# Optimization experiments

Hardware: AMD Instinct MI355X
Metric: run time of the kernel (lower is better)

The kernel has to match this reference:

```python
import jax, jax.numpy as jnp
import numpy as np

N, E = 50000, 800000
C_IN, C_OUT, DIM, K = 64, 64, 3, 2
EPS = 1e-5


def setup_inputs() -> dict:
    key = jax.random.key(0)
    k1, k2, k3, k4, k5 = jax.random.split(key, 5)
    x = jax.random.normal(k1, (N, C_IN), dtype=jnp.float32)
    edge_index = jax.random.randint(k2, (2, E), 0, N, dtype=jnp.int32)
    edge_attr = jax.random.uniform(k3, (E, DIM), dtype=jnp.float32)  # pseudo coords in [0,1]
    W = jax.random.normal(k4, (K ** DIM, C_IN, C_OUT), dtype=jnp.float32) * 0.05
    root = jax.random.normal(k5, (C_IN, C_OUT), dtype=jnp.float32) * 0.05
    gamma = jnp.ones((C_OUT,), dtype=jnp.float32)
    beta = jnp.zeros((C_OUT,), dtype=jnp.float32)
    return {"x": x, "edge_attr": edge_attr, "W": W, "root": root,
            "gamma": gamma, "beta": beta, "edge_index": edge_index}


def _spline_basis(edge_attr):
    """Degree-1 open B-spline basis. Returns (weights [E,2^D], kernel idx [E,2^D])."""
    D = edge_attr.shape[1]
    v = edge_attr * (K - 1)                      # [E, D]
    k0 = jnp.floor(v)
    frac = v - k0                                # in [0,1)
    k0 = k0.astype(jnp.int32)
    bits = np.stack(np.unravel_index(np.arange(2 ** D), (2,) * D), axis=-1).astype(np.int32)  # [2^D, D]
    bits_f = jnp.asarray(bits, dtype=edge_attr.dtype)
    # per-dim weight: frac if bit else (1 - frac); product over dims
    w = jnp.where(bits_f[None] > 0, frac[:, None, :], 1.0 - frac[:, None, :])  # [E, 2^D, D]
    weights = jnp.prod(w, axis=-1)               # [E, 2^D]
    idx_d = jnp.clip(k0[:, None, :] + bits[None], 0, K - 1)  # [E, 2^D, D]
    radix = jnp.asarray(K ** np.arange(D), dtype=jnp.int32)
    idx = jnp.sum(idx_d * radix, axis=-1)        # [E, 2^D] in [0, K^D)
    return weights, idx


def reference(x, edge_attr, W, root, gamma, beta, edge_index):
    src, dst = edge_index[0], edge_index[1]
    Etot = edge_attr.shape[0]
    S = W.shape[0]  # K^D

    weights, idx = _spline_basis(edge_attr)      # [E, 2^D] each
    # dense per-edge basis over all K^D kernel slots
    B = jnp.zeros((Etot, S), dtype=x.dtype).at[jnp.arange(Etot)[:, None], idx].add(weights)

    xj = x[src]                                  # [E, C_in] gather
    z = (B[:, :, None] * xj[:, None, :]).reshape(Etot, S * x.shape[1])  # [E, S*C_in]
    msg = z @ W.reshape(S * x.shape[1], W.shape[2])                     # [E, C_out]

    agg = jax.ops.segment_sum(msg, dst, num_segments=x.shape[0])        # scatter-add
    cnt = jax.ops.segment_sum(jnp.ones((Etot,), dtype=x.dtype), dst, num_segments=x.shape[0])
    out = agg / jnp.maximum(cnt, 1.0)[:, None] + x @ root               # mean aggr + root weight

    # BatchNorm over nodes (training-mode batch stats)
    mean = jnp.mean(out, axis=0)
    var = jnp.var(out, axis=0)
    y = (out - mean) * jax.lax.rsqrt(var + EPS) * gamma + beta
    return jax.nn.elu(y)
```

## Files before the change

kernel.cpp:

```cpp
#include <hip/hip_runtime.h>
#include <hip/hip_bf16.h>
#include <cstdint>
#include <cstddef>

#define NN 50000
#define NE 800000
#define EPS 1e-5f

typedef short bf16x8 __attribute__((ext_vector_type(8)));
typedef float f32x4  __attribute__((ext_vector_type(4)));
typedef float f32x2  __attribute__((ext_vector_type(2)));


#define NB_WT   144
#define NB_CNT  3125
#define NB_MFMA 1564
#define NB_SCAN 25

static __device__ __forceinline__ ushort f2bf(float f) {
    __hip_bfloat16 h = __float2bfloat16(f);
    return *reinterpret_cast<ushort*>(&h);
}
static __device__ __forceinline__ uint32_t pack2(float a, float b) {
    return (uint32_t)f2bf(a) | ((uint32_t)f2bf(b) << 16);
}

__global__ __launch_bounds__(256) void prep_count_k(const float* __restrict__ W,
                                                    const float* __restrict__ root,
                                                    ushort* __restrict__ WTg,
                                                    const int* __restrict__ ei,
                                                    int* __restrict__ deg,
                                                    int* __restrict__ rank) {
    const int b = blockIdx.x;
    if (b < NB_WT) {
        const int idx = b * 256 + threadIdx.x;
        const int s  = idx >> 12;
        const int co = (idx >> 6) & 63;
        const int ci = idx & 63;
        const float v = (s < 8) ? W[s * 4096 + ci * 64 + co] : root[ci * 64 + co];
        WTg[idx] = f2bf(v);
    } else {
        const int e = (b - NB_WT) * 256 + threadIdx.x;
        if (e < NE) rank[e] = atomicAdd(&deg[ei[NE + e]], 1);
    }
}

__global__ __launch_bounds__(256) void mfma_scan_k(
        const float* __restrict__ x, const ushort* __restrict__ WTg,
        uint8_t* __restrict__ H8, float* __restrict__ Hroot,
        const int* __restrict__ deg, int* __restrict__ offs,
        int* __restrict__ part) {
    __shared__ __align__(16) ushort XA[64 * 64];
    __shared__ __align__(16) ushort WT[5 * 64 * 64];
    __shared__ int sh[256];
    const int t = threadIdx.x;
    const int b = blockIdx.x;

    if (b >= NB_MFMA) {
        const int sb = b - NB_MFMA;
        const int base = sb * 2048 + t * 8;
        int v[8]; int sum = 0;
        #pragma unroll
        for (int k = 0; k < 8; ++k) {
            int i = base + k;
            int d = (i < NN) ? deg[i] : 0;
            v[k] = sum; sum += d;
        }
        sh[t] = sum; __syncthreads();
        for (int off = 1; off < 256; off <<= 1) {
            int val = sh[t];
            int add = (t >= off) ? sh[t - off] : 0;
            __syncthreads();
            sh[t] = val + add;
            __syncthreads();
        }
        int excl = (t > 0) ? sh[t - 1] : 0;
        #pragma unroll
        for (int k = 0; k < 8; ++k) {
            int i = base + k;
            if (i < NN) offs[i] = excl + v[k];
        }
        if (t == 255) part[sb] = sh[255];
        return;
    }

    const int bx   = (b < 782) ? b : b - 782;
    const int half = (b < 782) ? 0 : 1;
    const int n0 = bx * 64;
    const int sbeg   = half ? 5 : 0;
    const int scount = half ? 4 : 5;

    #pragma unroll
    for (int rep = 0; rep < 2; ++rep) {
        const int vt   = rep * 256 + t;
        const int row  = vt >> 3;
        const int col8 = vt & 7;
        const int n = n0 + row;
        uint4 u;
        if (n < NN) {
            const float4 v0 = *(const float4*)&x[(size_t)n * 64 + col8 * 8];
            const float4 v1 = *(const float4*)&x[(size_t)n * 64 + col8 * 8 + 4];
            u.x = pack2(v0.x, v0.y); u.y = pack2(v0.z, v0.w);
            u.z = pack2(v1.x, v1.y); u.w = pack2(v1.z, v1.w);
        } else {
            u = make_uint4(0, 0, 0, 0);
        }
        const int idx = (row * 64 + col8 * 8) ^ ((row & 7) << 3);
        *(uint4*)&XA[idx] = u;
    }
    const int nchunk = scount * 512;
    for (int c = t; c < nchunk; c += 256) {
        const int row  = c >> 3;
        const int col8 = c & 7;
        const uint4 u = *(const uint4*)&WTg[(size_t)(sbeg * 64 + row) * 64 + col8 * 8];
        const int idx = (row * 64 + col8 * 8) ^ ((row & 7) << 3);
        *(uint4*)&WT[idx] = u;
    }
    __syncthreads();

    const int w    = t >> 6;
    const int lane = t & 63;
    const int mrow = lane & 15;
    const int kgrp = lane >> 4;
    const int swz  = (mrow & 7) << 3;
    const int arow = w * 16 + mrow;
    const int n    = n0 + arow;

    const bf16x8 a0 = *(const bf16x8*)&XA[((arow * 64) + 0 * 32 + kgrp * 8) ^ swz];
    const bf16x8 a1 = *(const bf16x8*)&XA[((arow * 64) + 1 * 32 + kgrp * 8) ^ swz];

    for (int sl = 0; sl < scount; ++sl) {
        const int s = sbeg + sl;
        const ushort* wt = &WT[sl * 4096];
        f32x4 acc[4];
        #pragma unroll
        for (int ct = 0; ct < 4; ++ct) {
            acc[ct] = (f32x4){0.f, 0.f, 0.f, 0.f};
            const int brow = ct * 16 + mrow;
            const bf16x8 b0 = *(const bf16x8*)&wt[((brow * 64) + 0 * 32 + kgrp * 8) ^ swz];
            const bf16x8 b1 = *(const bf16x8*)&wt[((brow * 64) + 1 * 32 + kgrp * 8) ^ swz];
            acc[ct] = __builtin_amdgcn_mfma_f32_16x16x32_bf16(b0, a0, acc[ct], 0, 0, 0);
            acc[ct] = __builtin_amdgcn_mfma_f32_16x16x32_bf16(b1, a1, acc[ct], 0, 0, 0);
        }
        if (n < NN) {
            if (s < 8) {
                #pragma unroll
                for (int ct = 0; ct < 4; ++ct) {
                    int p = __builtin_amdgcn_cvt_pk_fp8_f32(acc[ct][0], acc[ct][1], 0, false);
                    p     = __builtin_amdgcn_cvt_pk_fp8_f32(acc[ct][2], acc[ct][3], p, true);
                    *(uint32_t*)&H8[(size_t)n * 512 + s * 64 + ct * 16 + kgrp * 4] = (uint32_t)p;
                }
            } else {
                #pragma unroll
                for (int ct = 0; ct < 4; ++ct) {
                    *(float4*)&Hroot[(size_t)n * 64 + ct * 16 + kgrp * 4] =
                        make_float4(acc[ct][0], acc[ct][1], acc[ct][2], acc[ct][3]);
                }
            }
        }
    }
}

__global__ __launch_bounds__(256) void scatter_k(const int* __restrict__ ei,
                                                 const float* __restrict__ attr,
                                                 const int* __restrict__ offs,
                                                 const int* __restrict__ part,
                                                 const int* __restrict__ rank,
                                                 int2* __restrict__ recs) {
    __shared__ int pp[25];
    const int t = threadIdx.x;
    if (t < 25) pp[t] = part[t];
    __syncthreads();
    if (t == 0) {
        int s = 0;
        #pragma unroll
        for (int i = 0; i < 25; ++i) { int v = pp[i]; pp[i] = s; s += v; }
    }
    __syncthreads();
    int e = blockIdx.x * 256 + t;
    if (e >= NE) return;
    const int src = ei[e];
    const int dst = ei[NE + e];
    const float f0 = attr[(size_t)e * 3 + 0];
    const float f1 = attr[(size_t)e * 3 + 1];
    const float f2 = attr[(size_t)e * 3 + 2];
    const uint32_t q = (uint32_t)rintf(f0 * 1023.f)
                     | ((uint32_t)rintf(f1 * 1023.f) << 10)
                     | ((uint32_t)rintf(f2 * 1023.f) << 20);
    const int p = offs[dst] + pp[dst >> 11] + rank[e];
    recs[p] = make_int2(src, (int)q);
}

__global__ __launch_bounds__(256) void aggregate_k(const int* __restrict__ offs,
                                                   const int* __restrict__ part,
                                                   const int* __restrict__ deg,
                                                   const int2* __restrict__ recs,
                                                   const uint8_t* __restrict__ H8,
                                                   const float* __restrict__ Hroot,
                                                   float* __restrict__ outb,
                                                   float* __restrict__ bnps,
                                                   float* __restrict__ bnpq) {
    __shared__ int pp[25];
    __shared__ float red_s[4][64], red_q[4][64];
    const int t = threadIdx.x, lane = t & 63, w = t >> 6;
    if (t < 25) pp[t] = part[t];
    __syncthreads();
    if (t == 0) {
        int s = 0;
        #pragma unroll
        for (int i = 0; i < 25; ++i) { int v = pp[i]; pp[i] = s; s += v; }
    }
    __syncthreads();

    const int n = blockIdx.x * 4 + w;
    const int sidx = lane >> 3;
    const int cog  = lane & 7;
    const float sg0 = (sidx & 1) ? 1.f : -1.f, cc0 = (sidx & 1) ? 0.f : 1.f;
    const float sg1 = (sidx & 2) ? 1.f : -1.f, cc1 = (sidx & 2) ? 0.f : 1.f;
    const float sg2 = (sidx & 4) ? 1.f : -1.f, cc2 = (sidx & 4) ? 0.f : 1.f;
    const int cnt = deg[n];
    const int beg = offs[n] + pp[n >> 11];
    const int2* rp = recs + beg;
    const size_t loff = (size_t)(lane << 3);

    f32x2 acc2[4] = {(f32x2){0.f, 0.f}, (f32x2){0.f, 0.f},
                     (f32x2){0.f, 0.f}, (f32x2){0.f, 0.f}};

#define DECODE_W(qv, wv)                                                     \
    {                                                                        \
        const uint32_t q_ = (uint32_t)(qv);                                  \
        const float f0_ = (float)(q_ & 1023u) * (1.f / 1023.f);              \
        const float f1_ = (float)((q_ >> 10) & 1023u) * (1.f / 1023.f);      \
        const float f2_ = (float)((q_ >> 20) & 1023u) * (1.f / 1023.f);      \
        wv = (cc0 + sg0 * f0_) * ((cc1 + sg1 * f1_) * (cc2 + sg2 * f2_));    \
    }
#define ACCUM(wv, h)                                                         \
    {                                                                        \
        const f32x2 w2_ = {wv, wv};                                          \
        acc2[0] += w2_ * (f32x2)__builtin_amdgcn_cvt_pk_f32_fp8((int)(h).x, false); \
        acc2[1] += w2_ * (f32x2)__builtin_amdgcn_cvt_pk_f32_fp8((int)(h).x, true);  \
        acc2[2] += w2_ * (f32x2)__builtin_amdgcn_cvt_pk_f32_fp8((int)(h).y, false); \
        acc2[3] += w2_ * (f32x2)__builtin_amdgcn_cvt_pk_f32_fp8((int)(h).y, true);  \
    }

    int j = 0;
    for (; j + 3 < cnt; j += 4) {
        const int2 r0 = rp[j];
        const int2 r1 = rp[j + 1];
        const int2 r2 = rp[j + 2];
        const int2 r3 = rp[j + 3];
        const uint2 h0 = *(const uint2*)(H8 + (size_t)r0.x * 512 + loff);
        const uint2 h1 = *(const uint2*)(H8 + (size_t)r1.x * 512 + loff);
        const uint2 h2 = *(const uint2*)(H8 + (size_t)r2.x * 512 + loff);
        const uint2 h3 = *(const uint2*)(H8 + (size_t)r3.x * 512 + loff);
        float w0, w1, w2, w3;
        DECODE_W(r0.y, w0); DECODE_W(r1.y, w1);
        DECODE_W(r2.y, w2); DECODE_W(r3.y, w3);
        ACCUM(w0, h0); ACCUM(w1, h1); ACCUM(w2, h2); ACCUM(w3, h3);
    }
    for (; j < cnt; ++j) {
        const int2 r0 = rp[j];
        const uint2 h0 = *(const uint2*)(H8 + (size_t)r0.x * 512 + loff);
        float w0;
        DECODE_W(r0.y, w0);
        ACCUM(w0, h0);
    }
#undef DECODE_W
#undef ACCUM

    float accf[8] = {acc2[0].x, acc2[0].y, acc2[1].x, acc2[1].y,
                     acc2[2].x, acc2[2].y, acc2[3].x, acc2[3].y};
    #pragma unroll
    for (int k = 0; k < 8; ++k) {
        float v = accf[k];
        v += __shfl_xor(v, 8, 64);
        v += __shfl_xor(v, 16, 64);
        v += __shfl_xor(v, 32, 64);
        accf[k] = v;
    }
    if (sidx == 0) {
        const float inv = 1.f / fmaxf((float)cnt, 1.f);
        const size_t base = (size_t)n * 64 + cog * 8;
        const float4 r0 = *(const float4*)&Hroot[base];
        const float4 r1 = *(const float4*)&Hroot[base + 4];
        float vv[8];
        vv[0] = accf[0] * inv + r0.x; vv[1] = accf[1] * inv + r0.y;
        vv[2] = accf[2] * inv + r0.z; vv[3] = accf[3] * inv + r0.w;
        vv[4] = accf[4] * inv + r1.x; vv[5] = accf[5] * inv + r1.y;
        vv[6] = accf[6] * inv + r1.z; vv[7] = accf[7] * inv + r1.w;
        *(float4*)&outb[base]     = make_float4(vv[0], vv[1], vv[2], vv[3]);
        *(float4*)&outb[base + 4] = make_float4(vv[4], vv[5], vv[6], vv[7]);
        #pragma unroll
        for (int k = 0; k < 8; ++k) {
            red_s[w][cog * 8 + k] = vv[k];
            red_q[w][cog * 8 + k] = vv[k] * vv[k];
        }
    }
    __syncthreads();
    if (t < 64) {
        const float s = red_s[0][t] + red_s[1][t] + red_s[2][t] + red_s[3][t];
        const float q = red_q[0][t] + red_q[1][t] + red_q[2][t] + red_q[3][t];
        const int slot = (blockIdx.x & 63) * 64 + t;
        atomicAdd(&bnps[slot], s);
        atomicAdd(&bnpq[slot], q);
    }
}

__global__ __launch_bounds__(256) void finalize_kernel(float* __restrict__ outb,
                                                       const float* __restrict__ bnps,
                                                       const float* __restrict__ bnpq,
                                                       const float* __restrict__ gamma,
                                                       const float* __restrict__ beta) {
    __shared__ float sc_sh[64], sh_sh[64];
    const int t = threadIdx.x;
    if (t < 64) {
        float s = 0.f, q = 0.f;
        for (int k = 0; k < 64; ++k) { s += bnps[k * 64 + t]; q += bnpq[k * 64 + t]; }
        const float mean = s * (1.f / NN);
        const float var  = q * (1.f / NN) - mean * mean;
        const float sc = rsqrtf(var + EPS) * gamma[t];
        sc_sh[t] = sc;
        sh_sh[t] = beta[t] - mean * sc;
    }
    __syncthreads();
    const int total4 = NN * 16;
    for (int idx = blockIdx.x * 256 + t; idx < total4; idx += gridDim.x * 256) {
        float4 v = ((const float4*)outb)[idx];
        const int co0 = (idx & 15) * 4;
        float o[4] = {v.x, v.y, v.z, v.w};
        #pragma unroll
        for (int j = 0; j < 4; ++j) {
            const float y = o[j] * sc_sh[co0 + j] + sh_sh[co0 + j];
            o[j] = (y > 0.f) ? y : expm1f(y);
        }
        ((float4*)outb)[idx] = make_float4(o[0], o[1], o[2], o[3]);
    }
}

extern "C" void kernel_launch(void* const* d_in, const int* in_sizes, int n_in,
                              void* d_out, int out_size, void* d_ws, size_t ws_size,
                              hipStream_t stream) {
    const float* x     = (const float*)d_in[0];
    const float* attr  = (const float*)d_in[1];
    const float* W     = (const float*)d_in[2];
    const float* root  = (const float*)d_in[3];
    const float* gamma = (const float*)d_in[4];
    const float* beta  = (const float*)d_in[5];
    const int*   ei    = (const int*)d_in[6];
    float* outb = (float*)d_out;

    char* ws = (char*)d_ws;
    uint8_t* H8    = (uint8_t*)(ws);
    float*   Hroot = (float*)(ws + 25600000);
    int2*    recs  = (int2*)(ws + 38400000);
    int*     rank  = (int*)(ws + 44800000);
    int*     offs  = (int*)(ws + 48000000);
    int*     deg   = (int*)(ws + 48200000);
    int*     part  = (int*)(ws + 48400000);
    float*   bnps  = (float*)(ws + 48400128);
    float*   bnpq  = (float*)(ws + 48416512);
    ushort*  WTg   = (ushort*)(ws + 48432896);

    hipMemsetAsync(ws + 48200000, 0, 232896, stream);

    prep_count_k<<<NB_WT + NB_CNT, 256, 0, stream>>>(W, root, WTg, ei, deg, rank);
    mfma_scan_k<<<NB_MFMA + NB_SCAN, 256, 0, stream>>>(x, WTg, H8, Hroot, deg, offs, part);
    scatter_k<<<NB_CNT, 256, 0, stream>>>(ei, attr, offs, part, rank, recs);
    aggregate_k<<<NN / 4, 256, 0, stream>>>(offs, part, deg, recs, H8, Hroot, outb, bnps, bnpq);
    finalize_kernel<<<256, 256, 0, stream>>>(outb, bnps, bnpq, gamma, beta);
}
```

Baseline: 175.3 us.

## Store root projection in bf16 and merge MFMA halves into one block

The x@root result is now stored as bf16 instead of fp32, which halves its write and read traffic between the MFMA and aggregate kernels. Each MFMA block now handles all 9 weight slices in two sequential passes that reload the shared weight tile, so x is loaded and converted only once per node tile, at the cost of half as many blocks. BatchNorm partial buffers are zeroed inside the prep kernel instead of by the memset, and the shared-memory reduction layout is transposed to reduce bank conflicts. Rounding the root term to bf16 adds a small amount of precision loss.

Measured after the change: 167.8 us. 4.3% less time.

```diff
diff --git a/kernel.cpp b/kernel.cpp
--- a/kernel.cpp
+++ b/kernel.cpp
@@ -14,12 +14,18 @@
 
 #define NB_WT   144
 #define NB_CNT  3125
-#define NB_MFMA 1564
+#define NB_MFMA 782
 #define NB_SCAN 25
 
 static __device__ __forceinline__ ushort f2bf(float f) {
     __hip_bfloat16 h = __float2bfloat16(f);
     return *reinterpret_cast<ushort*>(&h);
+}
+static __device__ __forceinline__ float bf_lo(uint32_t u) {
+    return __uint_as_float(u << 16);
+}
+static __device__ __forceinline__ float bf_hi(uint32_t u) {
+    return __uint_as_float(u & 0xffff0000u);
 }
 static __device__ __forceinline__ uint32_t pack2(float a, float b) {
     return (uint32_t)f2bf(a) | ((uint32_t)f2bf(b) << 16);
@@ -30,7 +36,9 @@
                                                     ushort* __restrict__ WTg,
                                                     const int* __restrict__ ei,
                                                     int* __restrict__ deg,
-                                                    int* __restrict__ rank) {
+                                                    int* __restrict__ rank,
+                                                    float* __restrict__ bnps,
+                                                    float* __restrict__ bnpq) {
     const int b = blockIdx.x;
     if (b < NB_WT) {
         const int idx = b * 256 + threadIdx.x;
@@ -39,6 +47,7 @@
         const int ci = idx & 63;
         const float v = (s < 8) ? W[s * 4096 + ci * 64 + co] : root[ci * 64 + co];
         WTg[idx] = f2bf(v);
+        if (idx < 4096) { bnps[idx] = 0.f; bnpq[idx] = 0.f; }
     } else {
         const int e = (b - NB_WT) * 256 + threadIdx.x;
         if (e < NE) rank[e] = atomicAdd(&deg[ei[NE + e]], 1);
@@ -47,7 +56,7 @@
 
 __global__ __launch_bounds__(256) void mfma_scan_k(
         const float* __restrict__ x, const ushort* __restrict__ WTg,
-        uint8_t* __restrict__ H8, float* __restrict__ Hroot,
+        uint8_t* __restrict__ H8, ushort* __restrict__ Hrootb,
         const int* __restrict__ deg, int* __restrict__ offs,
         int* __restrict__ part) {
     __shared__ __align__(16) ushort XA[64 * 64];
@@ -84,11 +93,7 @@
         return;
     }
 
-    const int bx   = (b < 782) ? b : b - 782;
-    const int half = (b < 782) ? 0 : 1;
-    const int n0 = bx * 64;
-    const int sbeg   = half ? 5 : 0;
-    const int scount = half ? 4 : 5;
+    const int n0 = b * 64;
 
     #pragma unroll
     for (int rep = 0; rep < 2; ++rep) {
@@ -108,15 +113,6 @@
         const int idx = (row * 64 + col8 * 8) ^ ((row & 7) << 3);
         *(uint4*)&XA[idx] = u;
     }
-    const int nchunk = scount * 512;
-    for (int c = t; c < nchunk; c += 256) {
-        const int row  = c >> 3;
-        const int col8 = c & 7;
-        const uint4 u = *(const uint4*)&WTg[(size_t)(sbeg * 64 + row) * 64 + col8 * 8];
-        const int idx = (row * 64 + col8 * 8) ^ ((row & 7) << 3);
-        *(uint4*)&WT[idx] = u;
-    }
-    __syncthreads();
 
     const int w    = t >> 6;
     const int lane = t & 63;
@@ -125,39 +121,57 @@
     const int swz  = (mrow & 7) << 3;
     const int arow = w * 16 + mrow;
     const int n    = n0 + arow;
-
-    const bf16x8 a0 = *(const bf16x8*)&XA[((arow * 64) + 0 * 32 + kgrp * 8) ^ swz];
-    const bf16x8 a1 = *(const bf16x8*)&XA[((arow * 64) + 1 * 32 + kgrp * 8) ^ swz];
-
-    for (int sl = 0; sl < scount; ++sl) {
-        const int s = sbeg + sl;
-        const ushort* wt = &WT[sl * 4096];
-        f32x4 acc[4];
-        #pragma unroll
-        for (int ct = 0; ct < 4; ++ct) {
-            acc[ct] = (f32x4){0.f, 0.f, 0.f, 0.f};
-            const int brow = ct * 16 + mrow;
-            const bf16x8 b0 = *(const bf16x8*)&wt[((brow * 64) + 0 * 32 + kgrp * 8) ^ swz];
-            const bf16x8 b1 = *(const bf16x8*)&wt[((brow * 64) + 1 * 32 + kgrp * 8) ^ swz];
-            acc[ct] = __builtin_amdgcn_mfma_f32_16x16x32_bf16(b0, a0, acc[ct], 0, 0, 0);
-            acc[ct] = __builtin_amdgcn_mfma_f32_16x16x32_bf16(b1, a1, acc[ct], 0, 0, 0);
-        }
-        if (n < NN) {
-            if (s < 8) {
-                #pragma unroll
-                for (int ct = 0; ct < 4; ++ct) {
-                    int p = __builtin_amdgcn_cvt_pk_fp8_f32(acc[ct][0], acc[ct][1], 0, false);
-                    p     = __builtin_amdgcn_cvt_pk_fp8_f32(acc[ct][2], acc[ct][3], p, true);
-                    *(uint32_t*)&H8[(size_t)n * 512 + s * 64 + ct * 16 + kgrp * 4] = (uint32_t)p;
-                }
-            } else {
-                #pragma unroll
-                for (int ct = 0; ct < 4; ++ct) {
-                    *(float4*)&Hroot[(size_t)n * 64 + ct * 16 + kgrp * 4] =
-                        make_float4(acc[ct][0], acc[ct][1], acc[ct][2], acc[ct][3]);
+    bf16x8 a0, a1;
+
+    for (int pass = 0; pass < 2; ++pass) {
+        const int sbeg   = pass ? 5 : 0;
+        const int scount = pass ? 4 : 5;
+        const int nchunk = scount * 512;
+        for (int c = t; c < nchunk; c += 256) {
+            const int row  = c >> 3;
+            const int col8 = c & 7;
+            const uint4 u = *(const uint4*)&WTg[(size_t)(sbeg * 64 + row) * 64 + col8 * 8];
+            const int idx = (row * 64 + col8 * 8) ^ ((row & 7) << 3);
+            *(uint4*)&WT[idx] = u;
+        }
+        __syncthreads();
+        if (pass == 0) {
+            a0 = *(const bf16x8*)&XA[((arow * 64) + 0 * 32 + kgrp * 8) ^ swz];
+            a1 = *(const bf16x8*)&XA[((arow * 64) + 1 * 32 + kgrp * 8) ^ swz];
+        }
+        for (int sl = 0; sl < scount; ++sl) {
+            const int s = sbeg + sl;
+            const ushort* wt = &WT[sl * 4096];
+            f32x4 acc[4];
+            #pragma unroll
+            for (int ct = 0; ct < 4; ++ct) {
+                acc[ct] = (f32x4){0.f, 0.f, 0.f, 0.f};
+                const int brow = ct * 16 + mrow;
+                const bf16x8 b0 = *(const bf16x8*)&wt[((brow * 64) + 0 * 32 + kgrp * 8) ^ swz];
+                const bf16x8 b1 = *(const bf16x8*)&wt[((brow * 64) + 1 * 32 + kgrp * 8) ^ swz];
+                acc[ct] = __builtin_amdgcn_mfma_f32_16x16x32_bf16(b0, a0, acc[ct], 0, 0, 0);
+                acc[ct] = __builtin_amdgcn_mfma_f32_16x16x32_bf16(b1, a1, acc[ct], 0, 0, 0);
+            }
+            if (n < NN) {
+                if (s < 8) {
+                    #pragma unroll
+                    for (int ct = 0; ct < 4; ++ct) {
+                        int p = __builtin_amdgcn_cvt_pk_fp8_f32(acc[ct][0], acc[ct][1], 0, false);
+                        p     = __builtin_amdgcn_cvt_pk_fp8_f32(acc[ct][2], acc[ct][3], p, true);
+                        *(uint32_t*)&H8[(size_t)n * 512 + s * 64 + ct * 16 + kgrp * 4] = (uint32_t)p;
+                    }
+                } else {
+                    #pragma unroll
+                    for (int ct = 0; ct < 4; ++ct) {
+                        ushort4 h4;
+                        h4.x = f2bf(acc[ct][0]); h4.y = f2bf(acc[ct][1]);
+                        h4.z = f2bf(acc[ct][2]); h4.w = f2bf(acc[ct][3]);
+                        *(ushort4*)&Hrootb[(size_t)n * 64 + ct * 16 + kgrp * 4] = h4;
+                    }
                 }
             }
         }
+        __syncthreads();
     }
 }
 
@@ -196,7 +210,7 @@
                                                    const int* __restrict__ deg,
                                                    const int2* __restrict__ recs,
                                                    const uint8_t* __restrict__ H8,
-                                                   const float* __restrict__ Hroot,
+                                                   const ushort* __restrict__ Hrootb,
                                                    float* __restrict__ outb,
                                                    float* __restrict__ bnps,
                                                    float* __restrict__ bnpq) {
@@ -281,26 +295,26 @@
     if (sidx == 0) {
         const float inv = 1.f / fmaxf((float)cnt, 1.f);
         const size_t base = (size_t)n * 64 + cog * 8;
-        const float4 r0 = *(const float4*)&Hroot[base];
-        const float4 r1 = *(const float4*)&Hroot[base + 4];
+        const uint4 hr = *(const uint4*)&Hrootb[base];
+        const float rr[8] = {bf_lo(hr.x), bf_hi(hr.x), bf_lo(hr.y), bf_hi(hr.y),
+                             bf_lo(hr.z), bf_hi(hr.z), bf_lo(hr.w), bf_hi(hr.w)};
         float vv[8];
-        vv[0] = accf[0] * inv + r0.x; vv[1] = accf[1] * inv + r0.y;
-        vv[2] = accf[2] * inv + r0.z; vv[3] = accf[3] * inv + r0.w;
-        vv[4] = accf[4] * inv + r1.x; vv[5] = accf[5] * inv + r1.y;
-        vv[6] = accf[6] * inv + r1.z; vv[7] = accf[7] * inv + r1.w;
+        #pragma unroll
+        for (int k = 0; k < 8; ++k) vv[k] = accf[k] * inv + rr[k];
         *(float4*)&outb[base]     = make_float4(vv[0], vv[1], vv[2], vv[3]);
         *(float4*)&outb[base + 4] = make_float4(vv[4], vv[5], vv[6], vv[7]);
         #pragma unroll
         for (int k = 0; k < 8; ++k) {
-            red_s[w][cog * 8 + k] = vv[k];
-            red_q[w][cog * 8 + k] = vv[k] * vv[k];
+            red_s[w][k * 8 + cog] = vv[k];
+            red_q[w][k * 8 + cog] = vv[k] * vv[k];
         }
     }
     __syncthreads();
     if (t < 64) {
         const float s = red_s[0][t] + red_s[1][t] + red_s[2][t] + red_s[3][t];
         const float q = red_q[0][t] + red_q[1][t] + red_q[2][t] + red_q[3][t];
-        const int slot = (blockIdx.x & 63) * 64 + t;
+        const int co = (t & 7) * 8 + (t >> 3);
+        const int slot = (blockIdx.x & 63) * 64 + co;
         atomicAdd(&bnps[slot], s);
         atomicAdd(&bnpq[slot], q);
     }
@@ -350,22 +364,22 @@
     float* outb = (float*)d_out;
 
     char* ws = (char*)d_ws;
-    uint8_t* H8    = (uint8_t*)(ws);
-    float*   Hroot = (float*)(ws + 25600000);
-    int2*    recs  = (int2*)(ws + 38400000);
-    int*     rank  = (int*)(ws + 44800000);
-    int*     offs  = (int*)(ws + 48000000);
-    int*     deg   = (int*)(ws + 48200000);
-    int*     part  = (int*)(ws + 48400000);
-    float*   bnps  = (float*)(ws + 48400128);
-    float*   bnpq  = (float*)(ws + 48416512);
-    ushort*  WTg   = (ushort*)(ws + 48432896);
-
-    hipMemsetAsync(ws + 48200000, 0, 232896, stream);
-
-    prep_count_k<<<NB_WT + NB_CNT, 256, 0, stream>>>(W, root, WTg, ei, deg, rank);
-    mfma_scan_k<<<NB_MFMA + NB_SCAN, 256, 0, stream>>>(x, WTg, H8, Hroot, deg, offs, part);
+    uint8_t* H8     = (uint8_t*)(ws);
+    ushort*  Hrootb = (ushort*)(ws + 25600000);
+    int2*    recs   = (int2*)(ws + 32000000);
+    int*     rank   = (int*)(ws + 38400000);
+    int*     offs   = (int*)(ws + 41600000);
+    int*     deg    = (int*)(ws + 41800000);
+    int*     part   = (int*)(ws + 42000000);
+    float*   bnps   = (float*)(ws + 42000128);
+    float*   bnpq   = (float*)(ws + 42016512);
+    ushort*  WTg    = (ushort*)(ws + 42032896);
+
+    hipMemsetAsync(ws + 41800000, 0, 200128, stream);
+
+    prep_count_k<<<NB_WT + NB_CNT, 256, 0, stream>>>(W, root, WTg, ei, deg, rank, bnps, bnpq);
+    mfma_scan_k<<<NB_MFMA + NB_SCAN, 256, 0, stream>>>(x, WTg, H8, Hrootb, deg, offs, part);
     scatter_k<<<NB_CNT, 256, 0, stream>>>(ei, attr, offs, part, rank, recs);
-    aggregate_k<<<NN / 4, 256, 0, stream>>>(offs, part, deg, recs, H8, Hroot, outb, bnps, bnpq);
+    aggregate_k<<<NN / 4, 256, 0, stream>>>(offs, part, deg, recs, H8, Hrootb, outb, bnps, bnpq);
     finalize_kernel<<<256, 256, 0, stream>>>(outb, bnps, bnpq, gamma, beta);
 }
```
